# Optimization experiments

Hardware: AMD Instinct MI355X
Metric: run time of the kernel (lower is better)

Reference implementation:

```python
import jax, jax.numpy as jnp
import numpy as np

DIM = 384
HEADS = 12
WIN = (2, 7, 7)
MLP_RATIO = 4.0
EPS = 1e-5


def _rel_index(Wt, Wh, Ww):
    t, h, w = np.meshgrid(np.arange(Wt), np.arange(Wh), np.arange(Ww), indexing='ij')
    coords = np.stack([t, h, w]).reshape(3, -1).T  # (N,3)
    rel = coords[:, None] - coords[None]  # (N,N,3)
    rel[..., 0] += Wt - 1
    rel[..., 1] += Wh - 1
    rel[..., 2] += Ww - 1
    rel[..., 0] *= (2 * Wh - 1) * (2 * Ww - 1)
    rel[..., 1] *= (2 * Ww - 1)
    return rel.sum(-1)  # (N,N) int


def setup_inputs() -> dict:
    key = jax.random.key(0)
    ks = jax.random.split(key, 16)
    d = DIM
    hdim = int(d * MLP_RATIO)
    Wt, Wh, Ww = WIN
    table_size = (2 * Wt - 1) * (2 * Wh - 1) * (2 * Ww - 1)
    s = lambda fan: 1.0 / np.sqrt(fan)
    return {
        'x': jax.random.normal(ks[0], (2, 8, 56, 56, d), jnp.float32),
        'norm1_g': jnp.ones((d,), jnp.float32),
        'norm1_b': jnp.zeros((d,), jnp.float32),
        'qkv_w': jax.random.normal(ks[1], (d, 3 * d), jnp.float32) * s(d),
        'qkv_b': jnp.zeros((3 * d,), jnp.float32),
        'proj_w': jax.random.normal(ks[2], (d, d), jnp.float32) * s(d),
        'proj_b': jnp.zeros((d,), jnp.float32),
        'bias_table': jax.random.normal(ks[3], (table_size, HEADS), jnp.float32) * 0.02,
        'norm2_g': jnp.ones((d,), jnp.float32),
        'norm2_b': jnp.zeros((d,), jnp.float32),
        'fc1_w': jax.random.normal(ks[4], (d, hdim), jnp.float32) * s(d),
        'fc1_b': jnp.zeros((hdim,), jnp.float32),
        'fc2_w': jax.random.normal(ks[5], (hdim, d), jnp.float32) * s(hdim),
        'fc2_b': jnp.zeros((d,), jnp.float32),
        'rel_index': jnp.asarray(_rel_index(*WIN), jnp.int32),
    }


def _ln(x, g, b):
    mu = x.mean(-1, keepdims=True)
    var = ((x - mu) ** 2).mean(-1, keepdims=True)
    return (x - mu) * jax.lax.rsqrt(var + EPS) * g + b


def _window_partition(x, win):
    B, T, H, W, C = x.shape
    Wt, Wh, Ww = win
    x = x.reshape(B, T // Wt, Wt, H // Wh, Wh, W // Ww, Ww, C)
    x = x.transpose(0, 1, 3, 5, 2, 4, 6, 7)
    return x.reshape(-1, Wt * Wh * Ww, C)


def _window_reverse(win_x, win, B, T, H, W):
    Wt, Wh, Ww = win
    C = win_x.shape[-1]
    x = win_x.reshape(B, T // Wt, H // Wh, W // Ww, Wt, Wh, Ww, C)
    x = x.transpose(0, 1, 4, 2, 5, 3, 6, 7)
    return x.reshape(B, T, H, W, C)


def reference(x, norm1_g, norm1_b, qkv_w, qkv_b, proj_w, proj_b, bias_table,
              norm2_g, norm2_b, fc1_w, fc1_b, fc2_w, fc2_b, rel_index):
    B, T, H, W, C = x.shape
    Wt, Wh, Ww = WIN
    N = Wt * Wh * Ww
    shift = (Wt // 2, Wh // 2, Ww // 2)
    head_dim = C // HEADS
    scale = head_dim ** -0.5

    shortcut = x
    h = _ln(x, norm1_g, norm1_b)
    h = jnp.roll(h, shift=(-shift[0], -shift[1], -shift[2]), axis=(1, 2, 3))
    # dims chosen divisible by window -> no padding branch
    wins = _window_partition(h, WIN)  # (BnW, N, C)
    BnW = wins.shape[0]

    qkv = wins @ qkv_w + qkv_b  # (BnW, N, 3C)
    qkv = qkv.reshape(BnW, N, 3, HEADS, head_dim).transpose(2, 0, 3, 1, 4)
    q, k, v = qkv[0] * scale, qkv[1], qkv[2]  # (BnW, H, N, d)

    bias = bias_table[rel_index.reshape(-1)].reshape(N, N, HEADS).transpose(2, 0, 1)
    attn = jnp.einsum('bhnd,bhmd->bhnm', q, k) + bias[None]
    attn = jax.nn.softmax(attn, axis=-1)
    out = jnp.einsum('bhnm,bhmd->bhnd', attn, v)
    out = out.transpose(0, 2, 1, 3).reshape(BnW, N, C)
    out = out @ proj_w + proj_b

    h = _window_reverse(out.reshape(-1, Wt, Wh, Ww, C), WIN, B, T, H, W)
    h = jnp.roll(h, shift=shift, axis=(1, 2, 3))
    x = shortcut + h

    h2 = _ln(x, norm2_g, norm2_b)
    h2 = jax.nn.gelu(h2 @ fc1_w + fc1_b, approximate=False) @ fc2_w + fc2_b
    return x + h2
```

## Files before the change

kernel.cpp:

```cpp
#include <hip/hip_runtime.h>
#include <cstdint>
#include <cstddef>


typedef __bf16 bf16x8 __attribute__((ext_vector_type(8)));
typedef __bf16 bf16x4 __attribute__((ext_vector_type(4)));
typedef float f32x4 __attribute__((ext_vector_type(4)));

#define DIM 384
#define QKV_DIM 1152
#define HID 1536
#define NHEADS 12
#define NTOK 50176
#define NWIN 512

__device__ __forceinline__ void gload16(const void* g, void* s) {
  __builtin_amdgcn_global_load_lds(
      (const __attribute__((address_space(1))) void*)g,
      (__attribute__((address_space(3))) void*)s, 16, 0, 0);
}

__global__ __launch_bounds__(256) void build_tokmap_k(int* __restrict__ map) {
  int t = blockIdx.x * 256 + threadIdx.x;
  if (t >= NTOK) return;
  int win = t / 98, n = t - win * 98;
  int b = win >> 8, tw = (win >> 6) & 3, hw = (win >> 3) & 7, ww = win & 7;
  int dt = n / 49; int rem = n - dt * 49; int dh = rem / 7, dw = rem - dh * 7;
  int t0 = (tw * 2 + dt + 1) & 7;
  int h0 = hw * 7 + dh + 3; if (h0 >= 56) h0 -= 56;
  int w0 = ww * 7 + dw + 3; if (w0 >= 56) w0 -= 56;
  map[t] = ((b * 8 + t0) * 56 + h0) * 56 + w0;
}

__global__ __launch_bounds__(256) void expand_biasp_k(const float* __restrict__ table,
                                                      const int* __restrict__ rel,
                                                      float* __restrict__ out) {
  int e = blockIdx.x * 256 + threadIdx.x;
  if (e >= NHEADS * 49 * 256) return;
  int r = e & 3, l = (e >> 2) & 63;
  int rest = e >> 8;
  int ni = rest % 7, mi = (rest / 7) % 7, h = rest / 49;
  int i = mi * 16 + (l >> 4) * 4 + r;
  int j = ni * 16 + (l & 15);
  float v;
  if (j >= 98) v = -1e30f;
  else if (i >= 98) v = 0.f;
  else v = table[rel[i * 98 + j] * NHEADS + h];
  out[e] = v;
}

__global__ __launch_bounds__(256) void pack_w_k(const float* __restrict__ W,
                                                __bf16* __restrict__ WP,
                                                int K, int N, int nk,
                                                int scaleCols, float scale) {
  int idx = blockIdx.x * 256 + threadIdx.x;
  if (idx >= (K * N) >> 3) return;
  int l = idx & 63, f = (idx >> 6) & 7;
  int rest = idx >> 9, kt = rest % nk, cn = rest / nk;
  int n = f >> 1, kk = f & 1;
  int col = cn * 64 + n * 16 + (l & 15);
  int k0 = kt * 64 + (kk * 4 + (l >> 4)) * 8;
  float sc = (col < scaleCols) ? scale : 1.0f;
  bf16x8 v;
  #pragma unroll
  for (int j = 0; j < 8; ++j)
    v[j] = (__bf16)(W[(size_t)(k0 + j) * N + col] * sc);
  *(bf16x8*)(WP + (size_t)idx * 8) = v;
}

__global__ __launch_bounds__(256) void scale_bias_k(const float* __restrict__ b,
                                                    float* __restrict__ out,
                                                    int n, int scaleCols, float scale) {
  int e = blockIdx.x * 256 + threadIdx.x;
  if (e >= n) return;
  out[e] = b[e] * (e < scaleCols ? scale : 1.0f);
}

__global__ __launch_bounds__(384) void vtrans_k(const __bf16* __restrict__ qkv,
                                                __bf16* __restrict__ vt) {
  __shared__ __align__(1024) char T[98304];
  int win = blockIdx.x, t = threadIdx.x;
  const __bf16* base = qkv + (size_t)win * 98 * QKV_DIM + 768 + t;
  #pragma unroll
  for (int c = 0; c < 16; ++c) {
    bf16x8 pk;
    #pragma unroll
    for (int e2 = 0; e2 < 8; ++e2) {
      int tok = c * 8 + e2;
      pk[e2] = (tok < 98) ? base[(size_t)tok * QKV_DIM] : (__bf16)0.f;
    }
    *(bf16x8*)(T + t * 256 + ((c ^ (t & 15)) << 4)) = pk;
  }
  __syncthreads();
  char* wb = (char*)(vt + (size_t)win * 49152);
  #pragma unroll
  for (int i = 0; i < 16; ++i) {
    int g = i * 6144 + t * 16;
    int row = g >> 8, p = (g >> 4) & 15;
    bf16x8 v = *(const bf16x8*)(T + row * 256 + (p << 4));
    int lc = p ^ (row & 15);
    *(bf16x8*)(wb + row * 256 + (lc << 4)) = v;
  }
}

template <typename T>
__global__ __launch_bounds__(256) void ln_k(const T* __restrict__ x,
                                            const float* __restrict__ g,
                                            const float* __restrict__ bta,
                                            __bf16* __restrict__ out,
                                            const int* __restrict__ map) {
  int w = threadIdx.x >> 6, l = threadIdx.x & 63;
  int tok = blockIdx.x * 4 + w;
  int src = map ? map[tok] : tok;
  const T* row = x + (size_t)src * DIM;
  float v[6]; float s = 0.f;
  #pragma unroll
  for (int j = 0; j < 6; ++j) { v[j] = (float)row[l + 64 * j]; s += v[j]; }
  #pragma unroll
  for (int m = 1; m < 64; m <<= 1) s += __shfl_xor(s, m, 64);
  float mu = s * (1.f / DIM);
  float var = 0.f;
  #pragma unroll
  for (int j = 0; j < 6; ++j) { float d = v[j] - mu; var += d * d; }
  #pragma unroll
  for (int m = 1; m < 64; m <<= 1) var += __shfl_xor(var, m, 64);
  float rs = rsqrtf(var * (1.f / DIM) + 1e-5f);
  __bf16* orow = out + (size_t)tok * DIM;
  #pragma unroll
  for (int j = 0; j < 6; ++j) {
    int c = l + 64 * j;
    orow[c] = (__bf16)((v[j] - mu) * rs * g[c] + bta[c]);
  }
}

template <int EPI>
__global__ __launch_bounds__(256) void gemm_k(const __bf16* __restrict__ A,
                                              const __bf16* __restrict__ WP,
                                              const float* __restrict__ bias,
                                              int M, int N, int K,
                                              __bf16* __restrict__ outb,
                                              float* __restrict__ outf,
                                              const float* __restrict__ residf,
                                              const __bf16* __restrict__ residb,
                                              const int* __restrict__ tokmap) {
  __shared__ __align__(1024) char lds[32768];
  const int tid = threadIdx.x;
  const int l = tid & 63, w = tid >> 6;
  const int lr = l & 15, lg = l >> 4;
  const int ntile = N >> 6;
  const int nwg = gridDim.x, qd = nwg >> 3, rm = nwg & 7;
  const int xcd = blockIdx.x & 7;
  const int wgid = (xcd < rm ? xcd * (qd + 1) : rm * (qd + 1) + (xcd - rm) * qd)
                   + (blockIdx.x >> 3);
  const int bm = wgid / ntile, bn = wgid - bm * ntile;
  const int m0 = (bm << 8) + (w << 6);
  const int n0 = bn << 6;
  const int nk = K >> 6;
  const int sch = (l & 7) ^ ((l >> 3) & 7);
  const __bf16* pa = A + (size_t)(m0 + (l >> 3)) * K + sch * 8;
  char* abuf = lds + (w << 13);
  const __bf16* pB = WP + (size_t)bn * nk * 4096 + l * 8;

#define STAGEA(kt)                                                   \
  {                                                                  \
    const size_t ko_ = (size_t)(kt) << 6;                            \
    _Pragma("unroll")                                                \
    for (int s_ = 0; s_ < 8; ++s_)                                   \
      gload16(pa + (size_t)(s_ * 8) * K + ko_, abuf + s_ * 1024);    \
  }
#define LOADB(kt)                                                    \
  {                                                                  \
    const __bf16* p_ = pB + (size_t)(kt) * 4096;                     \
    _Pragma("unroll")                                                \
    for (int f_ = 0; f_ < 8; ++f_)                                   \
      b[f_] = *(const bf16x8*)(p_ + f_ * 512);                       \
  }
#define LDA()                                                        \
  {                                                                  \
    _Pragma("unroll")                                                \
    for (int kk_ = 0; kk_ < 2; ++kk_) {                              \
      const int ck_ = (kk_ << 2) + lg;                               \
      _Pragma("unroll")                                              \
      for (int m_ = 0; m_ < 4; ++m_) {                               \
        int r_ = (m_ << 4) + lr;                                     \
        a[m_][kk_] = *(const bf16x8*)(abuf + (r_ << 7) +             \
                                      ((ck_ ^ (r_ & 7)) << 4));      \
      }                                                              \
    }                                                                \
    asm volatile("s_waitcnt lgkmcnt(0)" ::: "memory");               \
    __builtin_amdgcn_sched_barrier(0);                               \
  }

  bf16x8 a[4][2], b[8];
  f32x4 acc[4][4] = {};

  STAGEA(0)
  asm volatile("s_waitcnt vmcnt(0)" ::: "memory");
  LDA()

  for (int kt = 0; kt < nk; ++kt) {
    LOADB(kt)
    const bool pf = (kt + 1 < nk);
    if (pf) STAGEA(kt + 1)
    __builtin_amdgcn_s_setprio(1);
    #pragma unroll
    for (int kk = 0; kk < 2; ++kk)
      #pragma unroll
      for (int m = 0; m < 4; ++m)
        #pragma unroll
        for (int n = 0; n < 4; ++n)
          acc[m][n] = __builtin_amdgcn_mfma_f32_16x16x32_bf16(b[n * 2 + kk], a[m][kk],
                                                              acc[m][n], 0, 0, 0);
    __builtin_amdgcn_s_setprio(0);
    if (pf) {
      asm volatile("s_waitcnt vmcnt(0)" ::: "memory");
      LDA()
    }
  }
#undef STAGEA
#undef LOADB
#undef LDA

  if (EPI == 3) {
    #pragma unroll
    for (int hh = 0; hh < 2; ++hh) {
      #pragma unroll
      for (int m = 0; m < 4; ++m) {
        const int row = (m << 4) + lr;
        #pragma unroll
        for (int n2 = 0; n2 < 2; ++n2) {
          const int n = (hh << 1) + n2;
          const int gcol = n0 + (n << 4) + (lg << 2);
          f32x4 a4 = acc[m][n] + *(const f32x4*)(bias + gcol);
          const int ch = (n2 << 2) + lg;
          *(f32x4*)(abuf + (row << 7) + ((ch ^ (row & 7)) << 4)) = a4;
        }
      }
      asm volatile("s_waitcnt lgkmcnt(0)" ::: "memory");
      __builtin_amdgcn_sched_barrier(0);
      #pragma unroll
      for (int i = 0; i < 8; ++i) {
        const int row = (i << 3) + (l >> 3);
        const int p = (l & 7) ^ (row & 7);
        f32x4 v = *(const f32x4*)(abuf + (row << 7) + (p << 4));
        const int grow = m0 + row;
        const int gcol = n0 + (hh << 5) + ((l & 7) << 2);
        bf16x4 sv = *(const bf16x4*)(residb + (size_t)grow * N + gcol);
        f32x4 o;
        #pragma unroll
        for (int r = 0; r < 4; ++r) o[r] = v[r] + (float)sv[r];
        *(f32x4*)(outf + (size_t)grow * N + gcol) = o;
      }
      if (hh == 0) {
        asm volatile("s_waitcnt lgkmcnt(0)" ::: "memory");
        __builtin_amdgcn_sched_barrier(0);
      }
    }
  } else {
    #pragma unroll
    for (int m = 0; m < 4; ++m) {
      const int row = (m << 4) + lr;
      #pragma unroll
      for (int n = 0; n < 4; ++n) {
        const int gcol = n0 + (n << 4) + (lg << 2);
        f32x4 a4 = acc[m][n] + *(const f32x4*)(bias + gcol);
        bf16x4 c;
        if (EPI == 2) {
          #pragma unroll
          for (int r = 0; r < 4; ++r) {
            float vv = a4[r];
            float y = vv * (1.0f + 0.044715f * vv * vv);
            c[r] = (__bf16)(vv / (1.0f + __expf(-1.5957691216057308f * y)));
          }
        } else {
          #pragma unroll
          for (int r = 0; r < 4; ++r) c[r] = (__bf16)a4[r];
        }
        const int ch = (n << 1) + (lg >> 1);
        *(bf16x4*)(abuf + (row << 7) + ((ch ^ (row & 7)) << 4) + ((lg & 1) << 3)) = c;
      }
    }
    asm volatile("s_waitcnt lgkmcnt(0)" ::: "memory");
    __builtin_amdgcn_sched_barrier(0);
    #pragma unroll
    for (int i = 0; i < 8; ++i) {
      const int row = (i << 3) + (l >> 3);
      const int p = (l & 7) ^ (row & 7);
      bf16x8 v = *(const bf16x8*)(abuf + (row << 7) + (p << 4));
      const int gcol = n0 + ((l & 7) << 3);
      if (EPI == 1) {
        const int dst = tokmap[m0 + row];
        const float* rp = residf + (size_t)dst * N + gcol;
        f32x4 r0 = *(const f32x4*)rp, r1 = *(const f32x4*)(rp + 4);
        bf16x8 c2;
        #pragma unroll
        for (int j = 0; j < 4; ++j) {
          c2[j] = (__bf16)(r0[j] + (float)v[j]);
          c2[j + 4] = (__bf16)(r1[j] + (float)v[j + 4]);
        }
        *(bf16x8*)(outb + (size_t)dst * N + gcol) = c2;
      } else {
        *(bf16x8*)(outb + (size_t)(m0 + row) * N + gcol) = v;
      }
    }
  }
}

__global__ __launch_bounds__(64) void attn_k(const __bf16* __restrict__ qkv,
                                             const __bf16* __restrict__ vt,
                                             const float* __restrict__ pb,
                                             __bf16* __restrict__ out) {
  __shared__ __align__(1024) char P[4096];
  const int l = threadIdx.x, lr = l & 15, lg = l >> 4;
  const int bid = blockIdx.x;
  const int xc = bid & 7, kk = bid >> 3;
  const int wh = (kk / 7) * 8 + xc, mi = kk % 7;
  const int win = wh / NHEADS, h = wh - win * NHEADS;
  const size_t wbase = (size_t)win * 98 * QKV_DIM;
  const __bf16* qb = qkv + wbase + h * 32;
  const __bf16* kb = qb + 384;
  const bf16x8 z8 = {};
  const f32x4 fz = {};

  bf16x8 kf[7];
  #pragma unroll
  for (int ni = 0; ni < 7; ++ni) {
    int tok = ni * 16 + lr;
    kf[ni] = (tok < 98) ? *(const bf16x8*)(kb + (size_t)tok * QKV_DIM + lg * 8) : z8;
  }
  int qt = mi * 16 + lr;
  bf16x8 qf = (qt < 98) ? *(const bf16x8*)(qb + (size_t)qt * QKV_DIM + lg * 8) : z8;
  const f32x4* pbp = (const f32x4*)pb + (size_t)((h * 7 + mi) * 7) * 64 + l;
  f32x4 bv[7];
  #pragma unroll
  for (int ni = 0; ni < 7; ++ni) bv[ni] = pbp[ni * 64];

  f32x4 s[7];
  #pragma unroll
  for (int ni = 0; ni < 7; ++ni)
    s[ni] = __builtin_amdgcn_mfma_f32_16x16x32_bf16(qf, kf[ni], fz, 0, 0, 0);

  if (l < 32) {
    int row = l >> 1, c = 14 + (l & 1);
    *(f32x4*)(P + row * 256 + ((c ^ (row & 7)) << 4)) = fz;
  }

  #pragma unroll
  for (int r = 0; r < 4; ++r) {
    float mx = -1e30f;
    #pragma unroll
    for (int ni = 0; ni < 7; ++ni) {
      float vv = s[ni][r] + bv[ni][r];
      s[ni][r] = vv;
      mx = fmaxf(mx, vv);
    }
    #pragma unroll
    for (int m2 = 1; m2 < 16; m2 <<= 1) mx = fmaxf(mx, __shfl_xor(mx, m2, 64));
    float sum = 0.f;
    #pragma unroll
    for (int ni = 0; ni < 7; ++ni) { float p = __expf(s[ni][r] - mx); s[ni][r] = p; sum += p; }
    #pragma unroll
    for (int m2 = 1; m2 < 16; m2 <<= 1) sum += __shfl_xor(sum, m2, 64);
    float inv = 1.0f / sum;
    int il = lg * 4 + r;
    #pragma unroll
    for (int ni = 0; ni < 7; ++ni) {
      int j = ni * 16 + lr;
      *(__bf16*)(P + il * 256 + (((j >> 3) ^ (il & 7)) << 4) + ((j & 7) << 1)) =
          (__bf16)(s[ni][r] * inv);
    }
  }
  __syncthreads();

  bf16x8 pa[4];
  #pragma unroll
  for (int ks = 0; ks < 4; ++ks) {
    int ck = ks * 4 + lg;
    pa[ks] = *(const bf16x8*)(P + lr * 256 + ((ck ^ (lr & 7)) << 4));
  }
  const __bf16* vrow = vt + ((size_t)wh * 32) * 128;
  f32x4 oo[2];
  #pragma unroll
  for (int nf = 0; nf < 2; ++nf) {
    int d = nf * 16 + lr;
    f32x4 o = fz;
    #pragma unroll
    for (int ks = 0; ks < 4; ++ks) {
      bf16x8 vb = *(const bf16x8*)(vrow + (size_t)d * 128 + ks * 32 + lg * 8);
      o = __builtin_amdgcn_mfma_f32_16x16x32_bf16(pa[ks], vb, o, 0, 0, 0);
    }
    oo[nf] = o;
  }
  #pragma unroll
  for (int nf = 0; nf < 2; ++nf)
    #pragma unroll
    for (int r = 0; r < 4; ++r)
      *(__bf16*)(P + (lg * 4 + r) * 64 + (((nf << 4) + lr) << 1)) = (__bf16)oo[nf][r];
  asm volatile("s_waitcnt lgkmcnt(0)" ::: "memory");
  __builtin_amdgcn_sched_barrier(0);
  {
    const int row = l >> 2;
    bf16x8 v = *(const bf16x8*)(P + row * 64 + ((l & 3) << 4));
    const int tok = mi * 16 + row;
    if (tok < 98)
      *(bf16x8*)(out + ((size_t)win * 98 + tok) * DIM + h * 32 + ((l & 3) << 3)) = v;
  }
}

extern "C" void kernel_launch(void* const* d_in, const int* in_sizes, int n_in,
                              void* d_out, int out_size, void* d_ws, size_t ws_size,
                              hipStream_t stream) {
  const float* x      = (const float*)d_in[0];
  const float* n1g    = (const float*)d_in[1];
  const float* n1b    = (const float*)d_in[2];
  const float* qkv_w  = (const float*)d_in[3];
  const float* qkv_b  = (const float*)d_in[4];
  const float* proj_w = (const float*)d_in[5];
  const float* proj_b = (const float*)d_in[6];
  const float* btab   = (const float*)d_in[7];
  const float* n2g    = (const float*)d_in[8];
  const float* n2b    = (const float*)d_in[9];
  const float* fc1_w  = (const float*)d_in[10];
  const float* fc1_b  = (const float*)d_in[11];
  const float* fc2_w  = (const float*)d_in[12];
  const float* fc2_b  = (const float*)d_in[13];
  const int*   relidx = (const int*)d_in[14];
  float* outp = (float*)d_out;
  (void)in_sizes; (void)n_in; (void)out_size; (void)ws_size;

  char* ws = (char*)d_ws;
  size_t off = 0;
  auto alloc = [&](size_t bytes) {
    char* p = ws + off;
    off = (off + bytes + 255) & ~(size_t)255;
    return p;
  };
  int*    tokmap = (int*)alloc((size_t)NTOK * 4);
  float*  biasex = (float*)alloc((size_t)NHEADS * 49 * 256 * 4);
  __bf16* wqkvP  = (__bf16*)alloc((size_t)QKV_DIM * DIM * 2);
  __bf16* wprojP = (__bf16*)alloc((size_t)DIM * DIM * 2);
  __bf16* wfc1P  = (__bf16*)alloc((size_t)HID * DIM * 2);
  __bf16* wfc2P  = (__bf16*)alloc((size_t)DIM * HID * 2);
  float*  qkvbS  = (float*)alloc((size_t)QKV_DIM * 4);
  __bf16* tokens = (__bf16*)alloc((size_t)NTOK * DIM * 2);
  __bf16* qkvbuf = (__bf16*)alloc((size_t)NTOK * HID * 2);
  __bf16* s1     = (__bf16*)alloc((size_t)NTOK * DIM * 2);
  __bf16* attnout = tokens;
  __bf16* h1 = qkvbuf;
  __bf16* vt = (__bf16*)d_out;

  const float scale = 0.17677669529663687f;

  build_tokmap_k<<<NTOK / 256, 256, 0, stream>>>(tokmap);
  expand_biasp_k<<<(NHEADS * 49 * 256) / 256, 256, 0, stream>>>(btab, relidx, biasex);
  pack_w_k<<<(DIM * QKV_DIM / 8) / 256, 256, 0, stream>>>(qkv_w, wqkvP, DIM, QKV_DIM, 6, DIM, scale);
  pack_w_k<<<(DIM * DIM / 8) / 256, 256, 0, stream>>>(proj_w, wprojP, DIM, DIM, 6, 0, 1.0f);
  pack_w_k<<<(DIM * HID / 8) / 256, 256, 0, stream>>>(fc1_w, wfc1P, DIM, HID, 6, 0, 1.0f);
  pack_w_k<<<(HID * DIM / 8) / 256, 256, 0, stream>>>(fc2_w, wfc2P, HID, DIM, 24, 0, 1.0f);
  scale_bias_k<<<(QKV_DIM + 255) / 256, 256, 0, stream>>>(qkv_b, qkvbS, QKV_DIM, DIM, scale);

  ln_k<float><<<NTOK / 4, 256, 0, stream>>>(x, n1g, n1b, tokens, tokmap);
  gemm_k<0><<<(NTOK / 256) * (QKV_DIM / 64), 256, 0, stream>>>(
      tokens, wqkvP, qkvbS, NTOK, QKV_DIM, DIM, qkvbuf, nullptr, nullptr, nullptr, nullptr);
  vtrans_k<<<NWIN, 384, 0, stream>>>(qkvbuf, vt);
  attn_k<<<NWIN * NHEADS * 7, 64, 0, stream>>>(qkvbuf, vt, biasex, attnout);
  gemm_k<1><<<(NTOK / 256) * (DIM / 64), 256, 0, stream>>>(
      attnout, wprojP, proj_b, NTOK, DIM, DIM, s1, nullptr, x, nullptr, tokmap);
  ln_k<__bf16><<<NTOK / 4, 256, 0, stream>>>(s1, n2g, n2b, tokens, nullptr);
  gemm_k<2><<<(NTOK / 256) * (HID / 64), 256, 0, stream>>>(
      tokens, wfc1P, fc1_b, NTOK, HID, DIM, h1, nullptr, nullptr, nullptr, nullptr);
  gemm_k<3><<<(NTOK / 256) * (DIM / 64), 256, 0, stream>>>(
      h1, wfc2P, fc2_b, NTOK, DIM, HID, nullptr, outp, nullptr, s1, nullptr);
}
```

Measured before the change: 489.6 us.

## Emit LayerNorm output in MFMA fragment layout and stream GEMM operands from registers

The LayerNorm kernels now process 8 tokens per wave with vectorized loads and write their bf16 output directly in the packed MFMA fragment order. A new gemm_stream_k for the K=384 GEMMs (QKV and FC1) then loads both A and B fragments straight into registers with double-buffered prefetch, skipping LDS staging and the LDS read phase. gemm_k's now-unused EPI 2 branch and the non-residual store path are removed. The aim is to cut LDS traffic and synchronisation in the two largest-N GEMMs. The cost is higher register use from holding two full k-tiles of operands, and a second token buffer is allocated.

```diff
diff --git a/kernel.cpp b/kernel.cpp
--- a/kernel.cpp
+++ b/kernel.cpp
@@ -49,10 +49,10 @@
   out[e] = v;
 }
 
-__global__ __launch_bounds__(256) void pack_w_k(const float* __restrict__ W,
-                                                __bf16* __restrict__ WP,
-                                                int K, int N, int nk,
-                                                int scaleCols, float scale) {
+__global__ __launch_bounds__(256) void pack_w64_k(const float* __restrict__ W,
+                                                  __bf16* __restrict__ WP,
+                                                  int K, int N, int nk,
+                                                  int scaleCols, float scale) {
   int idx = blockIdx.x * 256 + threadIdx.x;
   if (idx >= (K * N) >> 3) return;
   int l = idx & 63, f = (idx >> 6) & 7;
@@ -103,33 +103,149 @@
   }
 }
 
-template <typename T>
-__global__ __launch_bounds__(256) void ln_k(const T* __restrict__ x,
-                                            const float* __restrict__ g,
-                                            const float* __restrict__ bta,
-                                            __bf16* __restrict__ out,
-                                            const int* __restrict__ map) {
-  int w = threadIdx.x >> 6, l = threadIdx.x & 63;
-  int tok = blockIdx.x * 4 + w;
-  int src = map ? map[tok] : tok;
+template <typename T, bool MAP>
+__global__ __launch_bounds__(256) void ln_pack_k(const T* __restrict__ x,
+                                                 const float* __restrict__ g,
+                                                 const float* __restrict__ bta,
+                                                 __bf16* __restrict__ outp,
+                                                 const int* __restrict__ map) {
+  const int w = threadIdx.x >> 6, l = threadIdx.x & 63;
+  const int tok = blockIdx.x * 32 + w * 8 + (l >> 3);
+  const int src = MAP ? map[tok] : tok;
   const T* row = x + (size_t)src * DIM;
-  float v[6]; float s = 0.f;
-  #pragma unroll
-  for (int j = 0; j < 6; ++j) { v[j] = (float)row[l + 64 * j]; s += v[j]; }
-  #pragma unroll
-  for (int m = 1; m < 64; m <<= 1) s += __shfl_xor(s, m, 64);
-  float mu = s * (1.f / DIM);
+  const int o0 = l & 7;
+  float v[6][8];
+  float s = 0.f;
+  #pragma unroll
+  for (int j = 0; j < 6; ++j) {
+    const int c = (o0 + 8 * j) * 8;
+    if constexpr (sizeof(T) == 4) {
+      f32x4 p0 = *(const f32x4*)(row + c);
+      f32x4 p1 = *(const f32x4*)(row + c + 4);
+      #pragma unroll
+      for (int e = 0; e < 4; ++e) { v[j][e] = p0[e]; v[j][e + 4] = p1[e]; }
+    } else {
+      bf16x8 p = *(const bf16x8*)(row + c);
+      #pragma unroll
+      for (int e = 0; e < 8; ++e) v[j][e] = (float)p[e];
+    }
+    #pragma unroll
+    for (int e = 0; e < 8; ++e) s += v[j][e];
+  }
+  s += __shfl_xor(s, 1, 64); s += __shfl_xor(s, 2, 64); s += __shfl_xor(s, 4, 64);
+  const float mu = s * (1.f / DIM);
   float var = 0.f;
   #pragma unroll
-  for (int j = 0; j < 6; ++j) { float d = v[j] - mu; var += d * d; }
-  #pragma unroll
-  for (int m = 1; m < 64; m <<= 1) var += __shfl_xor(var, m, 64);
-  float rs = rsqrtf(var * (1.f / DIM) + 1e-5f);
-  __bf16* orow = out + (size_t)tok * DIM;
+  for (int j = 0; j < 6; ++j)
+    #pragma unroll
+    for (int e = 0; e < 8; ++e) { float d = v[j][e] - mu; var += d * d; }
+  var += __shfl_xor(var, 1, 64); var += __shfl_xor(var, 2, 64); var += __shfl_xor(var, 4, 64);
+  const float rs = rsqrtf(var * (1.f / DIM) + 1e-5f);
+  const int mg = tok >> 6, m = (tok >> 4) & 3, lr = tok & 15;
+  const int kk = o0 >> 2, lg = o0 & 3;
+  __bf16* dst = outp + (size_t)mg * 24576 + (m * 2 + kk) * 512 + (lg * 16 + lr) * 8;
   #pragma unroll
   for (int j = 0; j < 6; ++j) {
-    int c = l + 64 * j;
-    orow[c] = (__bf16)((v[j] - mu) * rs * g[c] + bta[c]);
+    const int c = (o0 + 8 * j) * 8;
+    f32x4 g0 = *(const f32x4*)(g + c), g1 = *(const f32x4*)(g + c + 4);
+    f32x4 b0 = *(const f32x4*)(bta + c), b1 = *(const f32x4*)(bta + c + 4);
+    bf16x8 ov;
+    #pragma unroll
+    for (int e = 0; e < 4; ++e) {
+      ov[e] = (__bf16)((v[j][e] - mu) * rs * g0[e] + b0[e]);
+      ov[e + 4] = (__bf16)((v[j][e + 4] - mu) * rs * g1[e] + b1[e]);
+    }
+    *(bf16x8*)(dst + (size_t)j * 4096) = ov;
+  }
+}
+
+template <int EPI>
+__global__ __launch_bounds__(256) void gemm_stream_k(const __bf16* __restrict__ AP,
+                                                     const __bf16* __restrict__ WP,
+                                                     const float* __restrict__ bias,
+                                                     int N,
+                                                     __bf16* __restrict__ outb) {
+  __shared__ __align__(1024) char lds[32768];
+  const int tid = threadIdx.x;
+  const int l = tid & 63, w = tid >> 6;
+  const int lr = l & 15, lg = l >> 4;
+  const int ntile = N >> 6;
+  const int nwg = gridDim.x, qd = nwg >> 3, rm = nwg & 7;
+  const int xcd = blockIdx.x & 7;
+  const int wgid = (xcd < rm ? xcd * (qd + 1) : rm * (qd + 1) + (xcd - rm) * qd)
+                   + (blockIdx.x >> 3);
+  const int bm = wgid / ntile, bn = wgid - bm * ntile;
+  const int mg = bm * 4 + w;
+  const int m0 = mg << 6, n0 = bn << 6;
+  const __bf16* pA = AP + (size_t)mg * 24576 + l * 8;
+  const __bf16* pB = WP + (size_t)bn * 24576 + l * 8;
+
+  bf16x8 a[2][8], b[2][8];
+  f32x4 acc[4][4] = {};
+  #pragma unroll
+  for (int f = 0; f < 8; ++f) {
+    a[0][f] = *(const bf16x8*)(pA + f * 512);
+    b[0][f] = *(const bf16x8*)(pB + f * 512);
+  }
+  #pragma unroll
+  for (int kt = 0; kt < 6; ++kt) {
+    const int cur = kt & 1, nxt = cur ^ 1;
+    if (kt < 5) {
+      const size_t ko = (size_t)(kt + 1) * 4096;
+      #pragma unroll
+      for (int f = 0; f < 8; ++f) {
+        a[nxt][f] = *(const bf16x8*)(pA + ko + f * 512);
+        b[nxt][f] = *(const bf16x8*)(pB + ko + f * 512);
+      }
+      asm volatile("s_waitcnt vmcnt(16)" ::: "memory");
+    } else {
+      asm volatile("s_waitcnt vmcnt(0)" ::: "memory");
+    }
+    __builtin_amdgcn_sched_barrier(0);
+    __builtin_amdgcn_s_setprio(1);
+    #pragma unroll
+    for (int kk = 0; kk < 2; ++kk)
+      #pragma unroll
+      for (int m = 0; m < 4; ++m)
+        #pragma unroll
+        for (int n = 0; n < 4; ++n)
+          acc[m][n] = __builtin_amdgcn_mfma_f32_16x16x32_bf16(
+              b[cur][n * 2 + kk], a[cur][m * 2 + kk], acc[m][n], 0, 0, 0);
+    __builtin_amdgcn_s_setprio(0);
+  }
+
+  char* abuf = lds + (w << 13);
+  #pragma unroll
+  for (int m = 0; m < 4; ++m) {
+    const int row = (m << 4) + lr;
+    #pragma unroll
+    for (int n = 0; n < 4; ++n) {
+      const int gcol = n0 + (n << 4) + (lg << 2);
+      f32x4 a4 = acc[m][n] + *(const f32x4*)(bias + gcol);
+      bf16x4 c;
+      if (EPI == 2) {
+        #pragma unroll
+        for (int r = 0; r < 4; ++r) {
+          float vv = a4[r];
+          float y = vv * (1.0f + 0.044715f * vv * vv);
+          c[r] = (__bf16)(vv / (1.0f + __expf(-1.5957691216057308f * y)));
+        }
+      } else {
+        #pragma unroll
+        for (int r = 0; r < 4; ++r) c[r] = (__bf16)a4[r];
+      }
+      const int ch = (n << 1) + (lg >> 1);
+      *(bf16x4*)(abuf + (row << 7) + ((ch ^ (row & 7)) << 4) + ((lg & 1) << 3)) = c;
+    }
+  }
+  asm volatile("s_waitcnt lgkmcnt(0)" ::: "memory");
+  __builtin_amdgcn_sched_barrier(0);
+  #pragma unroll
+  for (int i = 0; i < 8; ++i) {
+    const int row = (i << 3) + (l >> 3);
+    const int p = (l & 7) ^ (row & 7);
+    bf16x8 v = *(const bf16x8*)(abuf + (row << 7) + (p << 4));
+    *(bf16x8*)(outb + (size_t)(m0 + row) * N + n0 + ((l & 7) << 3)) = v;
   }
 }
 
@@ -162,22 +278,17 @@
   const __bf16* pB = WP + (size_t)bn * nk * 4096 + l * 8;
 
 #define STAGEA(kt)                                                   \
-  {                                                                  \
-    const size_t ko_ = (size_t)(kt) << 6;                            \
+  { const size_t ko_ = (size_t)(kt) << 6;                            \
     _Pragma("unroll")                                                \
     for (int s_ = 0; s_ < 8; ++s_)                                   \
-      gload16(pa + (size_t)(s_ * 8) * K + ko_, abuf + s_ * 1024);    \
-  }
+      gload16(pa + (size_t)(s_ * 8) * K + ko_, abuf + s_ * 1024); }
 #define LOADB(kt)                                                    \
-  {                                                                  \
-    const __bf16* p_ = pB + (size_t)(kt) * 4096;                     \
+  { const __bf16* p_ = pB + (size_t)(kt) * 4096;                     \
     _Pragma("unroll")                                                \
     for (int f_ = 0; f_ < 8; ++f_)                                   \
-      b[f_] = *(const bf16x8*)(p_ + f_ * 512);                       \
-  }
+      b[f_] = *(const bf16x8*)(p_ + f_ * 512); }
 #define LDA()                                                        \
-  {                                                                  \
-    _Pragma("unroll")                                                \
+  { _Pragma("unroll")                                                \
     for (int kk_ = 0; kk_ < 2; ++kk_) {                              \
       const int ck_ = (kk_ << 2) + lg;                               \
       _Pragma("unroll")                                              \
@@ -185,19 +296,15 @@
         int r_ = (m_ << 4) + lr;                                     \
         a[m_][kk_] = *(const bf16x8*)(abuf + (r_ << 7) +             \
                                       ((ck_ ^ (r_ & 7)) << 4));      \
-      }                                                              \
-    }                                                                \
+      } }                                                            \
     asm volatile("s_waitcnt lgkmcnt(0)" ::: "memory");               \
-    __builtin_amdgcn_sched_barrier(0);                               \
-  }
+    __builtin_amdgcn_sched_barrier(0); }
 
   bf16x8 a[4][2], b[8];
   f32x4 acc[4][4] = {};
-
   STAGEA(0)
   asm volatile("s_waitcnt vmcnt(0)" ::: "memory");
   LDA()
-
   for (int kt = 0; kt < nk; ++kt) {
     LOADB(kt)
     const bool pf = (kt + 1 < nk);
@@ -265,17 +372,8 @@
         const int gcol = n0 + (n << 4) + (lg << 2);
         f32x4 a4 = acc[m][n] + *(const f32x4*)(bias + gcol);
         bf16x4 c;
-        if (EPI == 2) {
-          #pragma unroll
-          for (int r = 0; r < 4; ++r) {
-            float vv = a4[r];
-            float y = vv * (1.0f + 0.044715f * vv * vv);
-            c[r] = (__bf16)(vv / (1.0f + __expf(-1.5957691216057308f * y)));
-          }
-        } else {
-          #pragma unroll
-          for (int r = 0; r < 4; ++r) c[r] = (__bf16)a4[r];
-        }
+        #pragma unroll
+        for (int r = 0; r < 4; ++r) c[r] = (__bf16)a4[r];
         const int ch = (n << 1) + (lg >> 1);
         *(bf16x4*)(abuf + (row << 7) + ((ch ^ (row & 7)) << 4) + ((lg & 1) << 3)) = c;
       }
@@ -288,20 +386,16 @@
       const int p = (l & 7) ^ (row & 7);
       bf16x8 v = *(const bf16x8*)(abuf + (row << 7) + (p << 4));
       const int gcol = n0 + ((l & 7) << 3);
-      if (EPI == 1) {
-        const int dst = tokmap[m0 + row];
-        const float* rp = residf + (size_t)dst * N + gcol;
-        f32x4 r0 = *(const f32x4*)rp, r1 = *(const f32x4*)(rp + 4);
-        bf16x8 c2;
-        #pragma unroll
-        for (int j = 0; j < 4; ++j) {
-          c2[j] = (__bf16)(r0[j] + (float)v[j]);
-          c2[j + 4] = (__bf16)(r1[j] + (float)v[j + 4]);
-        }
-        *(bf16x8*)(outb + (size_t)dst * N + gcol) = c2;
-      } else {
-        *(bf16x8*)(outb + (size_t)(m0 + row) * N + gcol) = v;
-      }
+      const int dst = tokmap[m0 + row];
+      const float* rp = residf + (size_t)dst * N + gcol;
+      f32x4 r0 = *(const f32x4*)rp, r1 = *(const f32x4*)(rp + 4);
+      bf16x8 c2;
+      #pragma unroll
+      for (int j = 0; j < 4; ++j) {
+        c2[j] = (__bf16)(r0[j] + (float)v[j]);
+        c2[j + 4] = (__bf16)(r1[j] + (float)v[j + 4]);
+      }
+      *(bf16x8*)(outb + (size_t)dst * N + gcol) = c2;
     }
   }
 }
@@ -435,16 +529,17 @@
     off = (off + bytes + 255) & ~(size_t)255;
     return p;
   };
-  int*    tokmap = (int*)alloc((size_t)NTOK * 4);
-  float*  biasex = (float*)alloc((size_t)NHEADS * 49 * 256 * 4);
-  __bf16* wqkvP  = (__bf16*)alloc((size_t)QKV_DIM * DIM * 2);
-  __bf16* wprojP = (__bf16*)alloc((size_t)DIM * DIM * 2);
-  __bf16* wfc1P  = (__bf16*)alloc((size_t)HID * DIM * 2);
-  __bf16* wfc2P  = (__bf16*)alloc((size_t)DIM * HID * 2);
-  float*  qkvbS  = (float*)alloc((size_t)QKV_DIM * 4);
-  __bf16* tokens = (__bf16*)alloc((size_t)NTOK * DIM * 2);
-  __bf16* qkvbuf = (__bf16*)alloc((size_t)NTOK * HID * 2);
-  __bf16* s1     = (__bf16*)alloc((size_t)NTOK * DIM * 2);
+  int*    tokmap  = (int*)alloc((size_t)NTOK * 4);
+  float*  biasex  = (float*)alloc((size_t)NHEADS * 49 * 256 * 4);
+  __bf16* wqkvP   = (__bf16*)alloc((size_t)QKV_DIM * DIM * 2);
+  __bf16* wprojP  = (__bf16*)alloc((size_t)DIM * DIM * 2);
+  __bf16* wfc1P   = (__bf16*)alloc((size_t)HID * DIM * 2);
+  __bf16* wfc2P   = (__bf16*)alloc((size_t)DIM * HID * 2);
+  float*  qkvbS   = (float*)alloc((size_t)QKV_DIM * 4);
+  __bf16* tokens  = (__bf16*)alloc((size_t)NTOK * DIM * 2);
+  __bf16* qkvbuf  = (__bf16*)alloc((size_t)NTOK * HID * 2);
+  __bf16* s1      = (__bf16*)alloc((size_t)NTOK * DIM * 2);
+  __bf16* tokens2 = (__bf16*)alloc((size_t)NTOK * DIM * 2);
   __bf16* attnout = tokens;
   __bf16* h1 = qkvbuf;
   __bf16* vt = (__bf16*)d_out;
@@ -453,22 +548,22 @@
 
   build_tokmap_k<<<NTOK / 256, 256, 0, stream>>>(tokmap);
   expand_biasp_k<<<(NHEADS * 49 * 256) / 256, 256, 0, stream>>>(btab, relidx, biasex);
-  pack_w_k<<<(DIM * QKV_DIM / 8) / 256, 256, 0, stream>>>(qkv_w, wqkvP, DIM, QKV_DIM, 6, DIM, scale);
-  pack_w_k<<<(DIM * DIM / 8) / 256, 256, 0, stream>>>(proj_w, wprojP, DIM, DIM, 6, 0, 1.0f);
-  pack_w_k<<<(DIM * HID / 8) / 256, 256, 0, stream>>>(fc1_w, wfc1P, DIM, HID, 6, 0, 1.0f);
-  pack_w_k<<<(HID * DIM / 8) / 256, 256, 0, stream>>>(fc2_w, wfc2P, HID, DIM, 24, 0, 1.0f);
+  pack_w64_k<<<(DIM * QKV_DIM / 8) / 256, 256, 0, stream>>>(qkv_w, wqkvP, DIM, QKV_DIM, 6, DIM, scale);
+  pack_w64_k<<<(DIM * DIM / 8) / 256, 256, 0, stream>>>(proj_w, wprojP, DIM, DIM, 6, 0, 1.0f);
+  pack_w64_k<<<(DIM * HID / 8) / 256, 256, 0, stream>>>(fc1_w, wfc1P, DIM, HID, 6, 0, 1.0f);
+  pack_w64_k<<<(HID * DIM / 8) / 256, 256, 0, stream>>>(fc2_w, wfc2P, HID, DIM, 24, 0, 1.0f);
   scale_bias_k<<<(QKV_DIM + 255) / 256, 256, 0, stream>>>(qkv_b, qkvbS, QKV_DIM, DIM, scale);
 
-  ln_k<float><<<NTOK / 4, 256, 0, stream>>>(x, n1g, n1b, tokens, tokmap);
-  gemm_k<0><<<(NTOK / 256) * (QKV_DIM / 64), 256, 0, stream>>>(
-      tokens, wqkvP, qkvbS, NTOK, QKV_DIM, DIM, qkvbuf, nullptr, nullptr, nullptr, nullptr);
+  ln_pack_k<float, true><<<NTOK / 32, 256, 0, stream>>>(x, n1g, n1b, tokens, tokmap);
+  gemm_stream_k<0><<<(NTOK / 256) * (QKV_DIM / 64), 256, 0, stream>>>(
+      tokens, wqkvP, qkvbS, QKV_DIM, qkvbuf);
   vtrans_k<<<NWIN, 384, 0, stream>>>(qkvbuf, vt);
   attn_k<<<NWIN * NHEADS * 7, 64, 0, stream>>>(qkvbuf, vt, biasex, attnout);
   gemm_k<1><<<(NTOK / 256) * (DIM / 64), 256, 0, stream>>>(
       attnout, wprojP, proj_b, NTOK, DIM, DIM, s1, nullptr, x, nullptr, tokmap);
-  ln_k<__bf16><<<NTOK / 4, 256, 0, stream>>>(s1, n2g, n2b, tokens, nullptr);
-  gemm_k<2><<<(NTOK / 256) * (HID / 64), 256, 0, stream>>>(
-      tokens, wfc1P, fc1_b, NTOK, HID, DIM, h1, nullptr, nullptr, nullptr, nullptr);
+  ln_pack_k<__bf16, false><<<NTOK / 32, 256, 0, stream>>>(s1, n2g, n2b, tokens2, nullptr);
+  gemm_stream_k<2><<<(NTOK / 256) * (HID / 64), 256, 0, stream>>>(
+      tokens2, wfc1P, fc1_b, HID, h1);
   gemm_k<3><<<(NTOK / 256) * (DIM / 64), 256, 0, stream>>>(
       h1, wfc2P, fc2_b, NTOK, DIM, HID, nullptr, outp, nullptr, s1, nullptr);
 }
```

Result: faster. 472.6 us (-3.5%).
